# Kernel tuning notes

Hardware: AMD Instinct MI355X
Metric: run time of the kernel (lower is better)

## Reference

```python
import jax, jax.numpy as jnp
import numpy as np

N = 100000
E = 1600000
IN_FEATS = 128
N_HIDDEN = 128
N_CLASSES = 40
EPS = 1e-5


def _gconv(x, W, b, src, dst, n):
    # DGL GraphConv with norm='both': D_out^{-1/2} A D_in^{-1/2} X W (+ b), degrees clamped to >=1
    ones = jnp.ones(src.shape[0], x.dtype)
    out_deg = jnp.clip(jax.ops.segment_sum(ones, src, num_segments=n), 1.0)
    in_deg = jnp.clip(jax.ops.segment_sum(ones, dst, num_segments=n), 1.0)
    h = x * (out_deg ** -0.5)[:, None]
    agg = jax.ops.segment_sum(h[src], dst, num_segments=n)  # SpMM
    agg = agg * (in_deg ** -0.5)[:, None]
    out = agg @ W
    return out + b if b is not None else out


def setup_inputs() -> dict:
    key = jax.random.key(0)
    ks = jax.random.split(key, 16)
    s = lambda fan: 1.0 / np.sqrt(fan)
    feat = jax.random.normal(ks[0], (N, IN_FEATS), dtype=jnp.float32)
    src = jax.random.randint(ks[1], (E,), 0, N, dtype=jnp.int32)
    dst = jax.random.randint(ks[2], (E,), 0, N, dtype=jnp.int32)
    # backward convs: in_feats -> in_hidden (128->128 all layers); bias only at last layer
    Wb = jax.random.uniform(ks[3], (3, IN_FEATS, N_HIDDEN), jnp.float32, -s(IN_FEATS), s(IN_FEATS))
    bb2 = jax.random.uniform(ks[4], (N_HIDDEN,), jnp.float32, -s(IN_FEATS), s(IN_FEATS))
    # forward convs: layers 0,1 are 128->128, layer 2 is 128->40 with bias
    Wh01 = jax.random.uniform(ks[5], (2, N_HIDDEN, N_HIDDEN), jnp.float32, -s(N_HIDDEN), s(N_HIDDEN))
    W2 = jax.random.uniform(ks[6], (N_HIDDEN, N_CLASSES), jnp.float32, -s(N_HIDDEN), s(N_HIDDEN))
    b2 = jax.random.uniform(ks[7], (N_CLASSES,), jnp.float32, -s(N_HIDDEN), s(N_HIDDEN))
    # linear branch (use_linear=True), no bias
    Wl01 = jax.random.uniform(ks[8], (2, N_HIDDEN, N_HIDDEN), jnp.float32, -s(N_HIDDEN), s(N_HIDDEN))
    Wl2 = jax.random.uniform(ks[9], (N_HIDDEN, N_CLASSES), jnp.float32, -s(N_HIDDEN), s(N_HIDDEN))
    gamma = jnp.ones((2, N_HIDDEN), jnp.float32)
    beta = jnp.zeros((2, N_HIDDEN), jnp.float32)
    return {"feat": feat, "Wb": Wb, "bb2": bb2, "Wh01": Wh01, "W2": W2, "b2": b2,
            "Wl01": Wl01, "Wl2": Wl2, "gamma": gamma, "beta": beta, "src": src, "dst": dst}


def reference(feat, Wb, bb2, Wh01, W2, b2, Wl01, Wl2, gamma, beta, src, dst):
    n = feat.shape[0]
    h = feat  # dropout is identity in eval
    for i in range(3):
        last = i == 2
        # backward GraphConv on reversed graph, always applied to raw input features
        hb = _gconv(feat, Wb[i], bb2 if last else None, dst, src, n)
        h = jnp.maximum(h, hb)
        W = W2 if last else Wh01[i]
        Wl = Wl2 if last else Wl01[i]
        h = _gconv(h, W, b2 if last else None, src, dst, n) + h @ Wl
        if not last:
            mu = jnp.mean(h, axis=0)
            var = jnp.var(h, axis=0)
            h = (h - mu) * jax.lax.rsqrt(var + EPS) * gamma[i] + beta[i]
            h = jax.nn.relu(h)
    return h
```

## Files before the change

### kernel.cpp

```cpp
#include <hip/hip_runtime.h>

#define NN 100000
#define NE 1600000
#define KF 128
#define NCLS 40
#define EPSV 1e-5f
#define NBUK 391
#define TBUK 782
#define EPB 4096
#define P1B ((NE + EPB - 1) / EPB)
#define CAP 6144

typedef short bf16x8 __attribute__((ext_vector_type(8)));
typedef float f32x4 __attribute__((ext_vector_type(4)));
typedef unsigned short ushort;
typedef unsigned int uint;
typedef ushort ush8 __attribute__((ext_vector_type(8)));

static __device__ __forceinline__ int imax1(int x) { return x > 0 ? x : 1; }

static __device__ __forceinline__ ushort f2b(float f) {
  uint u = __builtin_bit_cast(uint, f);
  u += 0x7fffu + ((u >> 16) & 1u);
  return (ushort)(u >> 16);
}
static __device__ __forceinline__ float b2f(uint bits16) {
  return __builtin_bit_cast(float, bits16 << 16);
}


__global__ __launch_bounds__(256) void kb_hist(const int* __restrict__ src, const int* __restrict__ dst,
                                               int* __restrict__ gcount) {
  __shared__ int hist[TBUK];
  for (int t = threadIdx.x; t < TBUK; t += 256) hist[t] = 0;
  __syncthreads();
  int base = blockIdx.x * EPB + threadIdx.x;
#pragma unroll
  for (int i = 0; i < 16; ++i) {
    int e = base + i * 256;
    if (e < NE) {
      atomicAdd(&hist[dst[e] >> 8], 1);
      atomicAdd(&hist[NBUK + (src[e] >> 8)], 1);
    }
  }
  __syncthreads();
  for (int t = threadIdx.x; t < TBUK; t += 256)
    if (hist[t]) atomicAdd(&gcount[t], hist[t]);
}

__global__ __launch_bounds__(1024) void kb_scan(const int* __restrict__ gcount,
                                                int* __restrict__ gbase, int* __restrict__ gcur) {
  __shared__ int sm[1024];
  int t = threadIdx.x;
  int v = (t < TBUK) ? gcount[t] : 0;
  sm[t] = v;
  __syncthreads();
  for (int d = 1; d < 1024; d <<= 1) {
    int x = (t >= d) ? sm[t - d] : 0;
    __syncthreads();
    sm[t] += x;
    __syncthreads();
  }
  int excl = sm[t] - v;
  if (t <= TBUK) gbase[t] = excl;
  if (t < TBUK) gcur[t] = excl;
}

__global__ __launch_bounds__(256) void kb_place(const int* __restrict__ src, const int* __restrict__ dst,
                                                int* __restrict__ gcur,
                                                uint2* __restrict__ pairs_f, uint2* __restrict__ pairs_r) {
  __shared__ uint2 stage[EPB];
  __shared__ int hist[TBUK];
  __shared__ int sbase[TBUK];
  for (int t = threadIdx.x; t < TBUK; t += 256) hist[t] = 0;
  __syncthreads();
  int base = blockIdx.x * EPB;
  int nloc = min(EPB, NE - base);
  for (int i = threadIdx.x; i < nloc; i += 256) {
    int e = base + i;
    uint2 p;
    p.x = (uint)src[e];
    p.y = (uint)dst[e];
    stage[i] = p;
    atomicAdd(&hist[p.y >> 8], 1);
    atomicAdd(&hist[NBUK + (p.x >> 8)], 1);
  }
  __syncthreads();
  for (int t = threadIdx.x; t < TBUK; t += 256)
    sbase[t] = hist[t] ? atomicAdd(&gcur[t], hist[t]) : 0;
  __syncthreads();
  for (int i = threadIdx.x; i < nloc; i += 256) {
    uint2 p = stage[i];
    int pf = atomicAdd(&sbase[p.y >> 8], 1);
    int pr = atomicAdd(&sbase[NBUK + (p.x >> 8)], 1);
    pairs_f[pf] = make_uint2(p.y, p.x);
    pairs_r[pr - NE] = make_uint2(p.x, p.y);
  }
}

__global__ __launch_bounds__(256) void kb_build(const uint2* __restrict__ pairs_f,
                                                const uint2* __restrict__ pairs_r,
                                                const int* __restrict__ gbase,
                                                int* __restrict__ idx_f, int* __restrict__ idx_r,
                                                int* __restrict__ ptr_f, int* __restrict__ ptr_r,
                                                int* __restrict__ deg_in, int* __restrict__ deg_out) {
  __shared__ uint2 stage[CAP];
  __shared__ int deg[256];
  __shared__ int ss[256];
  __shared__ int cur[256];
  int b = blockIdx.x;
  int rev = (int)(b >= NBUK);
  int k = b - rev * NBUK;
  const uint2* pairs = rev ? pairs_r : pairs_f;
  int* idx = rev ? idx_r : idx_f;
  int* ptr = rev ? ptr_r : ptr_f;
  int* degA = rev ? deg_out : deg_in;
  int gb = gbase[b];
  int cnt = gbase[b + 1] - gb;
  int base = gb - rev * NE;
  int lo = k << 8;
  int t = threadIdx.x;
  deg[t] = 0;
  __syncthreads();
  for (int i = t; i < cnt; i += 256) {
    uint2 p = pairs[base + i];
    if (i < CAP) stage[i] = p;
    atomicAdd(&deg[(int)p.x - lo], 1);
  }
  __syncthreads();
  int dv = deg[t];
  if (lo + t < NN) degA[lo + t] = dv;
  ss[t] = dv;
  __syncthreads();
  for (int d = 1; d < 256; d <<= 1) {
    int x = (t >= d) ? ss[t - d] : 0;
    __syncthreads();
    ss[t] += x;
    __syncthreads();
  }
  int ex = ss[t] - dv;
  if (lo + t < NN) ptr[lo + t] = base + ex;
  cur[t] = ex;
  if (b == NBUK - 1 && t == 0) ptr_f[NN] = NE;
  if (b == TBUK - 1 && t == 0) ptr_r[NN] = NE;
  __syncthreads();
  for (int i = t; i < cnt; i += 256) {
    uint2 p = (i < CAP) ? stage[i] : pairs[base + i];
    int pos = atomicAdd(&cur[(int)p.x - lo], 1);
    idx[base + pos] = (int)p.y;
  }
}

__global__ void k_rsq(const int* __restrict__ deg_out, const int* __restrict__ deg_in,
                      float* __restrict__ ro, float* __restrict__ ri) {
  int i = blockIdx.x * blockDim.x + threadIdx.x;
  if (i < NN) {
    ro[i] = rsqrtf((float)imax1(deg_out[i]));
    ri[i] = rsqrtf((float)imax1(deg_in[i]));
  }
}

__global__ __launch_bounds__(256) void k_convF(const float* __restrict__ in, const float* __restrict__ ri,
                       ushort* __restrict__ out) {
  int t = blockIdx.x * blockDim.x + threadIdx.x;
  int i = t * 8;
  float w = ri[t >> 4];
  float4 a = *(const float4*)(in + i);
  float4 b = *(const float4*)(in + i + 4);
  ush8 o;
  o[0] = f2b(a.x * w); o[1] = f2b(a.y * w); o[2] = f2b(a.z * w); o[3] = f2b(a.w * w);
  o[4] = f2b(b.x * w); o[5] = f2b(b.y * w); o[6] = f2b(b.z * w); o[7] = f2b(b.w * w);
  *(ush8*)(out + i) = o;
}

#define WT_W2 (7 * 16384)
#define WT_L2 (WT_W2 + NCLS * KF)
__global__ __launch_bounds__(256) void k_convW(const float* __restrict__ Wb, const float* __restrict__ Wh01,
                       const float* __restrict__ Wl01, const float* __restrict__ W2,
                       const float* __restrict__ Wl2, ushort* __restrict__ wt) {
  int i = blockIdx.x * blockDim.x + threadIdx.x;
  float v;
  if (i < WT_W2) {
    int m = i >> 14, r = (i >> 7) & 127, k = i & 127;
    const float* srcm = (m < 3) ? (Wb + m * 16384)
                      : (m < 5) ? (Wh01 + (m - 3) * 16384)
                                : (Wl01 + (m - 5) * 16384);
    v = srcm[k * KF + r];
  } else {
    int j = i - WT_W2;
    int m2 = j / (NCLS * KF);
    int t = j - m2 * (NCLS * KF);
    int n = t >> 7, k = t & 127;
    v = (m2 ? Wl2 : W2)[k * NCLS + n];
  }
  wt[i] = f2b(v);
}

__global__ __launch_bounds__(256) void k_spmm_b(const ushort* __restrict__ in,
                      const int* __restrict__ ptr, const int* __restrict__ idx,
                      const float* __restrict__ wout, ushort* __restrict__ out) {
  int wid = (blockIdx.x * blockDim.x + threadIdx.x) >> 6;
  int lane = threadIdx.x & 63;
  if (wid >= NN) return;
  int beg = ptr[wid], end = ptr[wid + 1];
  int strm = lane >> 4;
  int c8 = (lane & 15) * 8;
  float s[8];
#pragma unroll
  for (int j = 0; j < 8; ++j) s[j] = 0.f;
  int p = beg + strm;
  for (; p + 4 < end; p += 8) {
    int u0 = idx[p], u1 = idx[p + 4];
    uint4 v0 = *(const uint4*)(in + (size_t)u0 * KF + c8);
    uint4 v1 = *(const uint4*)(in + (size_t)u1 * KF + c8);
    s[0] += b2f(v0.x & 0xffffu) + b2f(v1.x & 0xffffu);
    s[1] += b2f(v0.x >> 16)     + b2f(v1.x >> 16);
    s[2] += b2f(v0.y & 0xffffu) + b2f(v1.y & 0xffffu);
    s[3] += b2f(v0.y >> 16)     + b2f(v1.y >> 16);
    s[4] += b2f(v0.z & 0xffffu) + b2f(v1.z & 0xffffu);
    s[5] += b2f(v0.z >> 16)     + b2f(v1.z >> 16);
    s[6] += b2f(v0.w & 0xffffu) + b2f(v1.w & 0xffffu);
    s[7] += b2f(v0.w >> 16)     + b2f(v1.w >> 16);
  }
  if (p < end) {
    int u0 = idx[p];
    uint4 v0 = *(const uint4*)(in + (size_t)u0 * KF + c8);
    s[0] += b2f(v0.x & 0xffffu);
    s[1] += b2f(v0.x >> 16);
    s[2] += b2f(v0.y & 0xffffu);
    s[3] += b2f(v0.y >> 16);
    s[4] += b2f(v0.z & 0xffffu);
    s[5] += b2f(v0.z >> 16);
    s[6] += b2f(v0.w & 0xffffu);
    s[7] += b2f(v0.w >> 16);
  }
#pragma unroll
  for (int j = 0; j < 8; ++j) {
    s[j] += __shfl_xor(s[j], 16);
    s[j] += __shfl_xor(s[j], 32);
  }
  if (lane < 16) {
    float w = wout[wid];
    ush8 o;
#pragma unroll
    for (int j = 0; j < 8; ++j) o[j] = f2b(s[j] * w);
    *(ush8*)(out + (size_t)wid * KF + c8) = o;
  }
}

template <int NCT, bool DUAL, int EPI, bool HASB, bool NORMP>
__global__ __launch_bounds__(256) void k_gemm(
    const ushort* __restrict__ A1, const ushort* __restrict__ Wt1,
    const ushort* __restrict__ A2, const ushort* __restrict__ Wt2,
    const float* __restrict__ bias, const void* __restrict__ hprev,
    const float* __restrict__ ab, const float* __restrict__ rosc,
    float* __restrict__ outf, ushort* __restrict__ outb, ushort* __restrict__ outs,
    float* __restrict__ stat) {
  int lane = threadIdx.x & 63;
  int w = threadIdx.x >> 6;
  int r0 = blockIdx.x * 64 + w * 16;
  int arow = r0 + (lane & 15);
  if (arow > NN - 1) arow = NN - 1;
  int k0 = (lane >> 4) * 8;

  bf16x8 a1[4], a2[4];
#pragma unroll
  for (int ks = 0; ks < 4; ++ks) {
    a1[ks] = *(const bf16x8*)(A1 + (size_t)arow * KF + ks * 32 + k0);
    if (DUAL) a2[ks] = *(const bf16x8*)(A2 + (size_t)arow * KF + ks * 32 + k0);
  }
  f32x4 acc[NCT];
#pragma unroll
  for (int ct = 0; ct < NCT; ++ct) acc[ct] = (f32x4){0.f, 0.f, 0.f, 0.f};

#pragma unroll
  for (int ks = 0; ks < 4; ++ks) {
#pragma unroll
    for (int ct = 0; ct < NCT; ++ct) {
      int ncol = ct * 16 + (lane & 15);
      if (EPI == 2 && ncol > NCLS - 1) ncol = NCLS - 1;
      bf16x8 b1 = *(const bf16x8*)(Wt1 + (size_t)ncol * KF + ks * 32 + k0);
      acc[ct] = __builtin_amdgcn_mfma_f32_16x16x32_bf16(a1[ks], b1, acc[ct], 0, 0, 0);
      if (DUAL) {
        bf16x8 b2 = *(const bf16x8*)(Wt2 + (size_t)ncol * KF + ks * 32 + k0);
        acc[ct] = __builtin_amdgcn_mfma_f32_16x16x32_bf16(a2[ks], b2, acc[ct], 0, 0, 0);
      }
    }
  }

  int rbase = r0 + (lane >> 4) * 4;
  if constexpr (EPI == 0) {
    float rsc[4];
#pragma unroll
    for (int j = 0; j < 4; ++j) rsc[j] = rosc[min(rbase + j, NN - 1)];
#pragma unroll
    for (int ct = 0; ct < NCT; ++ct) {
      int col = ct * 16 + (lane & 15);
#pragma unroll
      for (int j = 0; j < 4; ++j) {
        int rr = rbase + j;
        if (rr >= NN) continue;
        float v = acc[ct][j];
        if (HASB) v += bias[col];
        float p;
        if (NORMP)
          p = fmaxf(0.f, b2f((uint)((const ushort*)hprev)[(size_t)rr * KF + col]) * ab[col] + ab[KF + col]);
        else
          p = ((const float*)hprev)[(size_t)rr * KF + col];
        float hv = fmaxf(p, v);
        outb[(size_t)rr * KF + col] = f2b(hv);
        outs[(size_t)rr * KF + col] = f2b(hv * rsc[j]);
      }
    }
  } else if constexpr (EPI == 1) {
    __shared__ float smS[4][128];
    __shared__ float smQ[4][128];
    float colS[NCT], colQ[NCT];
#pragma unroll
    for (int ct = 0; ct < NCT; ++ct) { colS[ct] = 0.f; colQ[ct] = 0.f; }
#pragma unroll
    for (int ct = 0; ct < NCT; ++ct) {
      int col = ct * 16 + (lane & 15);
#pragma unroll
      for (int j = 0; j < 4; ++j) {
        int rr = rbase + j;
        if (rr >= NN) continue;
        float v = acc[ct][j];
        outb[(size_t)rr * KF + col] = f2b(v);
        colS[ct] += v;
        colQ[ct] += v * v;
      }
    }
#pragma unroll
    for (int ct = 0; ct < NCT; ++ct) {
      colS[ct] += __shfl_xor(colS[ct], 16);
      colS[ct] += __shfl_xor(colS[ct], 32);
      colQ[ct] += __shfl_xor(colQ[ct], 16);
      colQ[ct] += __shfl_xor(colQ[ct], 32);
    }
    if (lane < 16) {
#pragma unroll
      for (int ct = 0; ct < NCT; ++ct) {
        smS[w][ct * 16 + lane] = colS[ct];
        smQ[w][ct * 16 + lane] = colQ[ct];
      }
    }
    __syncthreads();
    int tid = threadIdx.x;
    if (tid < 128)
      atomicAdd(&stat[tid], smS[0][tid] + smS[1][tid] + smS[2][tid] + smS[3][tid]);
    else
      atomicAdd(&stat[tid], smQ[0][tid - 128] + smQ[1][tid - 128] + smQ[2][tid - 128] + smQ[3][tid - 128]);
  } else {
#pragma unroll
    for (int ct = 0; ct < NCT; ++ct) {
      int col = ct * 16 + (lane & 15);
#pragma unroll
      for (int j = 0; j < 4; ++j) {
        int rr = rbase + j;
        if (rr >= NN) continue;
        if (col < NCLS) outf[(size_t)rr * NCLS + col] = acc[ct][j] + bias[col];
      }
    }
  }
}

__global__ void k_stats_fin(const float* __restrict__ stat, const float* __restrict__ gamma,
                            const float* __restrict__ beta, float* __restrict__ ab) {
  int c = threadIdx.x;
  float s = stat[c], q = stat[128 + c];
  float mu = s / (float)NN;
  float var = q / (float)NN - mu * mu;
  float rs = rsqrtf(var + EPSV);
  float a = gamma[c] * rs;
  ab[c] = a;
  ab[KF + c] = beta[c] - mu * a;
}

extern "C" void kernel_launch(void* const* d_in, const int* in_sizes, int n_in,
                              void* d_out, int out_size, void* d_ws, size_t ws_size,
                              hipStream_t stream) {
  const float* feat  = (const float*)d_in[0];
  const float* Wb    = (const float*)d_in[1];
  const float* bb2   = (const float*)d_in[2];
  const float* Wh01  = (const float*)d_in[3];
  const float* W2    = (const float*)d_in[4];
  const float* b2    = (const float*)d_in[5];
  const float* Wl01  = (const float*)d_in[6];
  const float* Wl2   = (const float*)d_in[7];
  const float* gamma = (const float*)d_in[8];
  const float* beta  = (const float*)d_in[9];
  const int* src = (const int*)d_in[10];
  const int* dst = (const int*)d_in[11];
  float* out = (float*)d_out;

  char* ws = (char*)d_ws;
  size_t off = 0;
  auto alloc = [&](size_t b) { size_t o = off; off += (b + 255) & ~(size_t)255; return o; };
  size_t z0 = alloc((size_t)(TBUK + 512) * 4);
  int* gcount = (int*)(ws + z0);
  float* stat = (float*)(gcount + TBUK);
  int* gbase = (int*)(ws + alloc((size_t)(TBUK + 1) * 4));
  int* gcur  = (int*)(ws + alloc((size_t)TBUK * 4));
  int* deg_out = (int*)(ws + alloc((size_t)NN * 4));
  int* deg_in  = (int*)(ws + alloc((size_t)NN * 4));
  int* ptr_f = (int*)(ws + alloc((size_t)(NN + 1) * 4));
  int* ptr_r = (int*)(ws + alloc((size_t)(NN + 1) * 4));
  int* idx_f = (int*)(ws + alloc((size_t)NE * 4));
  int* idx_r = (int*)(ws + alloc((size_t)NE * 4));
  uint2* pairs_f = (uint2*)(ws + alloc((size_t)NE * 8));
  uint2* pairs_r = (uint2*)(ws + alloc((size_t)NE * 8));
  float* ro = (float*)(ws + alloc((size_t)NN * 4));
  float* ri = (float*)(ws + alloc((size_t)NN * 4));
  ushort* featb = (ushort*)(ws + alloc((size_t)NN * KF * 2));
  ushort* aggb  = (ushort*)(ws + alloc((size_t)NN * KF * 2));
  ushort* hmaxb = (ushort*)(ws + alloc((size_t)NN * KF * 2));
  ushort* hmaxs = (ushort*)(ws + alloc((size_t)NN * KF * 2));
  float* ab = (float*)(ws + alloc((size_t)256 * 4));
  ushort* wt = (ushort*)(ws + alloc((size_t)(WT_L2 + NCLS * KF) * 2));
  ushort* t1b = featb;
  (void)ws_size;

  hipMemsetAsync(ws + z0, 0, (size_t)(TBUK + 512) * 4, stream);
  kb_hist<<<P1B, 256, 0, stream>>>(src, dst, gcount);
  kb_scan<<<1, 1024, 0, stream>>>(gcount, gbase, gcur);
  kb_place<<<P1B, 256, 0, stream>>>(src, dst, gcur, pairs_f, pairs_r);
  kb_build<<<TBUK, 256, 0, stream>>>(pairs_f, pairs_r, gbase, idx_f, idx_r,
                                     ptr_f, ptr_r, deg_in, deg_out);
  k_rsq<<<(NN + 255) / 256, 256, 0, stream>>>(deg_out, deg_in, ro, ri);
  k_convW<<<(WT_L2 + NCLS * KF + 255) / 256, 256, 0, stream>>>(Wb, Wh01, Wl01, W2, Wl2, wt);
  k_convF<<<NN * KF / 8 / 256, 256, 0, stream>>>(feat, ri, featb);

  const ushort* wtB[3] = {wt, wt + 16384, wt + 2 * 16384};
  const ushort* wtH[2] = {wt + 3 * 16384, wt + 4 * 16384};
  const ushort* wtL[2] = {wt + 5 * 16384, wt + 6 * 16384};
  const ushort* wtW2 = wt + WT_W2;
  const ushort* wtL2 = wt + WT_L2;

  int sb = (NN * 64 + 255) / 256;
  k_spmm_b<<<sb, 256, 0, stream>>>(featb, ptr_r, idx_r, ro, aggb);

  int mb = (NN + 63) / 64;
  k_gemm<8, false, 0, false, false><<<mb, 256, 0, stream>>>(
      aggb, wtB[0], nullptr, nullptr, nullptr, feat, nullptr, ro, nullptr, hmaxb, hmaxs, nullptr);
  k_spmm_b<<<sb, 256, 0, stream>>>(hmaxs, ptr_f, idx_f, ri, t1b);
  k_gemm<8, true, 1, false, false><<<mb, 256, 0, stream>>>(
      t1b, wtH[0], hmaxb, wtL[0], nullptr, nullptr, nullptr, nullptr, nullptr, hmaxb, nullptr, stat);
  k_stats_fin<<<1, 128, 0, stream>>>(stat, gamma, beta, ab);
  k_gemm<8, false, 0, false, true><<<mb, 256, 0, stream>>>(
      aggb, wtB[1], nullptr, nullptr, nullptr, hmaxb, ab, ro, nullptr, hmaxb, hmaxs, nullptr);
  k_spmm_b<<<sb, 256, 0, stream>>>(hmaxs, ptr_f, idx_f, ri, t1b);
  k_gemm<8, true, 1, false, false><<<mb, 256, 0, stream>>>(
      t1b, wtH[1], hmaxb, wtL[1], nullptr, nullptr, nullptr, nullptr, nullptr, hmaxb, nullptr, stat + 256);
  k_stats_fin<<<1, 128, 0, stream>>>(stat + 256, gamma + KF, beta + KF, ab);
  k_gemm<8, false, 0, true, true><<<mb, 256, 0, stream>>>(
      aggb, wtB[2], nullptr, nullptr, bb2, hmaxb, ab, ro, nullptr, hmaxb, hmaxs, nullptr);
  k_spmm_b<<<sb, 256, 0, stream>>>(hmaxs, ptr_f, idx_f, ri, t1b);
  k_gemm<3, true, 2, false, false><<<mb, 256, 0, stream>>>(
      t1b, wtW2, hmaxb, wtL2, b2, nullptr, nullptr, nullptr, out, nullptr, nullptr, nullptr);
}
```

Before: 821.7 us.

## Split GEMM waves across output columns and keep weight fragments in registers

The dense GEMM kernel is restructured so each of the four waves in a block covers all 64 rows but only a 32-column slice, rather than 16 rows across every column. Each wave loads its weight fragments once into registers and reuses them for four row tiles, cutting repeated weight loads. The A tiles are now read by all four waves. Because waves in a block now write rows that other waves still read as their second input, a separate hpreb buffer holds the pre-norm activations to avoid that race. For the 40-class output, half the waves do clamped work whose results are thrown away.

```diff
diff --git a/kernel.cpp b/kernel.cpp
--- a/kernel.cpp
+++ b/kernel.cpp
@@ -248,7 +248,7 @@
   }
 }
 
-template <int NCT, bool DUAL, int EPI, bool HASB, bool NORMP>
+template <int WCT, bool DUAL, int EPI, bool HASB, bool NORMP>
 __global__ __launch_bounds__(256) void k_gemm(
     const ushort* __restrict__ A1, const ushort* __restrict__ Wt1,
     const ushort* __restrict__ A2, const ushort* __restrict__ Wt2,
@@ -258,81 +258,100 @@
     float* __restrict__ stat) {
   int lane = threadIdx.x & 63;
   int w = threadIdx.x >> 6;
-  int r0 = blockIdx.x * 64 + w * 16;
-  int arow = r0 + (lane & 15);
-  if (arow > NN - 1) arow = NN - 1;
+  int r0 = blockIdx.x * 64;
+  int wcol = w * (WCT * 16);
   int k0 = (lane >> 4) * 8;
-
-  bf16x8 a1[4], a2[4];
-#pragma unroll
-  for (int ks = 0; ks < 4; ++ks) {
-    a1[ks] = *(const bf16x8*)(A1 + (size_t)arow * KF + ks * 32 + k0);
-    if (DUAL) a2[ks] = *(const bf16x8*)(A2 + (size_t)arow * KF + ks * 32 + k0);
-  }
-  f32x4 acc[NCT];
-#pragma unroll
-  for (int ct = 0; ct < NCT; ++ct) acc[ct] = (f32x4){0.f, 0.f, 0.f, 0.f};
-
-#pragma unroll
-  for (int ks = 0; ks < 4; ++ks) {
-#pragma unroll
-    for (int ct = 0; ct < NCT; ++ct) {
-      int ncol = ct * 16 + (lane & 15);
-      if (EPI == 2 && ncol > NCLS - 1) ncol = NCLS - 1;
-      bf16x8 b1 = *(const bf16x8*)(Wt1 + (size_t)ncol * KF + ks * 32 + k0);
-      acc[ct] = __builtin_amdgcn_mfma_f32_16x16x32_bf16(a1[ks], b1, acc[ct], 0, 0, 0);
-      if (DUAL) {
-        bf16x8 b2 = *(const bf16x8*)(Wt2 + (size_t)ncol * KF + ks * 32 + k0);
-        acc[ct] = __builtin_amdgcn_mfma_f32_16x16x32_bf16(a2[ks], b2, acc[ct], 0, 0, 0);
+  int l15 = lane & 15;
+  int g = lane >> 4;
+
+  bf16x8 b1[WCT][4];
+  bf16x8 b2[DUAL ? WCT : 1][DUAL ? 4 : 1];
+#pragma unroll
+  for (int ct = 0; ct < WCT; ++ct) {
+    int ncol = wcol + ct * 16 + l15;
+    if (EPI == 2) ncol = min(ncol, NCLS - 1);
+#pragma unroll
+    for (int ks = 0; ks < 4; ++ks) {
+      b1[ct][ks] = *(const bf16x8*)(Wt1 + (size_t)ncol * KF + ks * 32 + k0);
+      if (DUAL) b2[ct][ks] = *(const bf16x8*)(Wt2 + (size_t)ncol * KF + ks * 32 + k0);
+    }
+  }
+
+  f32x4 acc[4][WCT];
+#pragma unroll
+  for (int rt = 0; rt < 4; ++rt)
+#pragma unroll
+    for (int ct = 0; ct < WCT; ++ct) acc[rt][ct] = (f32x4){0.f, 0.f, 0.f, 0.f};
+
+#pragma unroll
+  for (int rt = 0; rt < 4; ++rt) {
+    int arow = min(r0 + rt * 16 + l15, NN - 1);
+    bf16x8 a1[4], a2[DUAL ? 4 : 1];
+#pragma unroll
+    for (int ks = 0; ks < 4; ++ks) {
+      a1[ks] = *(const bf16x8*)(A1 + (size_t)arow * KF + ks * 32 + k0);
+      if (DUAL) a2[ks] = *(const bf16x8*)(A2 + (size_t)arow * KF + ks * 32 + k0);
+    }
+#pragma unroll
+    for (int ks = 0; ks < 4; ++ks)
+#pragma unroll
+      for (int ct = 0; ct < WCT; ++ct) {
+        acc[rt][ct] = __builtin_amdgcn_mfma_f32_16x16x32_bf16(a1[ks], b1[ct][ks], acc[rt][ct], 0, 0, 0);
+        if (DUAL)
+          acc[rt][ct] = __builtin_amdgcn_mfma_f32_16x16x32_bf16(a2[ks], b2[ct][ks], acc[rt][ct], 0, 0, 0);
       }
-    }
-  }
-
-  int rbase = r0 + (lane >> 4) * 4;
+  }
+
   if constexpr (EPI == 0) {
-    float rsc[4];
-#pragma unroll
-    for (int j = 0; j < 4; ++j) rsc[j] = rosc[min(rbase + j, NN - 1)];
-#pragma unroll
-    for (int ct = 0; ct < NCT; ++ct) {
-      int col = ct * 16 + (lane & 15);
+#pragma unroll
+    for (int rt = 0; rt < 4; ++rt) {
+      int rbase = r0 + rt * 16 + g * 4;
 #pragma unroll
       for (int j = 0; j < 4; ++j) {
         int rr = rbase + j;
         if (rr >= NN) continue;
-        float v = acc[ct][j];
-        if (HASB) v += bias[col];
-        float p;
-        if (NORMP)
-          p = fmaxf(0.f, b2f((uint)((const ushort*)hprev)[(size_t)rr * KF + col]) * ab[col] + ab[KF + col]);
-        else
-          p = ((const float*)hprev)[(size_t)rr * KF + col];
-        float hv = fmaxf(p, v);
-        outb[(size_t)rr * KF + col] = f2b(hv);
-        outs[(size_t)rr * KF + col] = f2b(hv * rsc[j]);
+        float rs = rosc[rr];
+#pragma unroll
+        for (int ct = 0; ct < WCT; ++ct) {
+          int col = wcol + ct * 16 + l15;
+          float v = acc[rt][ct][j];
+          if (HASB) v += bias[col];
+          float p;
+          if (NORMP)
+            p = fmaxf(0.f, b2f((uint)((const ushort*)hprev)[(size_t)rr * KF + col]) * ab[col] + ab[KF + col]);
+          else
+            p = ((const float*)hprev)[(size_t)rr * KF + col];
+          float hv = fmaxf(p, v);
+          outb[(size_t)rr * KF + col] = f2b(hv);
+          outs[(size_t)rr * KF + col] = f2b(hv * rs);
+        }
       }
     }
   } else if constexpr (EPI == 1) {
-    __shared__ float smS[4][128];
-    __shared__ float smQ[4][128];
-    float colS[NCT], colQ[NCT];
-#pragma unroll
-    for (int ct = 0; ct < NCT; ++ct) { colS[ct] = 0.f; colQ[ct] = 0.f; }
-#pragma unroll
-    for (int ct = 0; ct < NCT; ++ct) {
-      int col = ct * 16 + (lane & 15);
-#pragma unroll
-      for (int j = 0; j < 4; ++j) {
-        int rr = rbase + j;
-        if (rr >= NN) continue;
-        float v = acc[ct][j];
-        outb[(size_t)rr * KF + col] = f2b(v);
-        colS[ct] += v;
-        colQ[ct] += v * v;
+    __shared__ float smS[128];
+    __shared__ float smQ[128];
+    float colS[WCT], colQ[WCT];
+#pragma unroll
+    for (int ct = 0; ct < WCT; ++ct) { colS[ct] = 0.f; colQ[ct] = 0.f; }
+#pragma unroll
+    for (int rt = 0; rt < 4; ++rt) {
+      int rbase = r0 + rt * 16 + g * 4;
+#pragma unroll
+      for (int ct = 0; ct < WCT; ++ct) {
+        int col = wcol + ct * 16 + l15;
+#pragma unroll
+        for (int j = 0; j < 4; ++j) {
+          int rr = rbase + j;
+          if (rr >= NN) continue;
+          float v = acc[rt][ct][j];
+          outb[(size_t)rr * KF + col] = f2b(v);
+          colS[ct] += v;
+          colQ[ct] += v * v;
+        }
       }
     }
 #pragma unroll
-    for (int ct = 0; ct < NCT; ++ct) {
+    for (int ct = 0; ct < WCT; ++ct) {
       colS[ct] += __shfl_xor(colS[ct], 16);
       colS[ct] += __shfl_xor(colS[ct], 32);
       colQ[ct] += __shfl_xor(colQ[ct], 16);
@@ -340,26 +359,31 @@
     }
     if (lane < 16) {
 #pragma unroll
-      for (int ct = 0; ct < NCT; ++ct) {
-        smS[w][ct * 16 + lane] = colS[ct];
-        smQ[w][ct * 16 + lane] = colQ[ct];
+      for (int ct = 0; ct < WCT; ++ct) {
+        smS[wcol + ct * 16 + lane] = colS[ct];
+        smQ[wcol + ct * 16 + lane] = colQ[ct];
       }
     }
     __syncthreads();
     int tid = threadIdx.x;
     if (tid < 128)
-      atomicAdd(&stat[tid], smS[0][tid] + smS[1][tid] + smS[2][tid] + smS[3][tid]);
+      atomicAdd(&stat[tid], smS[tid]);
     else
-      atomicAdd(&stat[tid], smQ[0][tid - 128] + smQ[1][tid - 128] + smQ[2][tid - 128] + smQ[3][tid - 128]);
+      atomicAdd(&stat[tid], smQ[tid - 128]);
   } else {
 #pragma unroll
-    for (int ct = 0; ct < NCT; ++ct) {
-      int col = ct * 16 + (lane & 15);
-#pragma unroll
-      for (int j = 0; j < 4; ++j) {
-        int rr = rbase + j;
-        if (rr >= NN) continue;
-        if (col < NCLS) outf[(size_t)rr * NCLS + col] = acc[ct][j] + bias[col];
+    for (int rt = 0; rt < 4; ++rt) {
+      int rbase = r0 + rt * 16 + g * 4;
+#pragma unroll
+      for (int ct = 0; ct < WCT; ++ct) {
+        int col = wcol + ct * 16 + l15;
+        if (col >= NCLS) continue;
+#pragma unroll
+        for (int j = 0; j < 4; ++j) {
+          int rr = rbase + j;
+          if (rr >= NN) continue;
+          outf[(size_t)rr * NCLS + col] = acc[rt][ct][j] + bias[col];
+        }
       }
     }
   }
@@ -416,6 +440,7 @@
   ushort* aggb  = (ushort*)(ws + alloc((size_t)NN * KF * 2));
   ushort* hmaxb = (ushort*)(ws + alloc((size_t)NN * KF * 2));
   ushort* hmaxs = (ushort*)(ws + alloc((size_t)NN * KF * 2));
+  ushort* hpreb = (ushort*)(ws + alloc((size_t)NN * KF * 2));
   float* ab = (float*)(ws + alloc((size_t)256 * 4));
   ushort* wt = (ushort*)(ws + alloc((size_t)(WT_L2 + NCLS * KF) * 2));
   ushort* t1b = featb;
@@ -441,21 +466,21 @@
   k_spmm_b<<<sb, 256, 0, stream>>>(featb, ptr_r, idx_r, ro, aggb);
 
   int mb = (NN + 63) / 64;
-  k_gemm<8, false, 0, false, false><<<mb, 256, 0, stream>>>(
+  k_gemm<2, false, 0, false, false><<<mb, 256, 0, stream>>>(
       aggb, wtB[0], nullptr, nullptr, nullptr, feat, nullptr, ro, nullptr, hmaxb, hmaxs, nullptr);
   k_spmm_b<<<sb, 256, 0, stream>>>(hmaxs, ptr_f, idx_f, ri, t1b);
-  k_gemm<8, true, 1, false, false><<<mb, 256, 0, stream>>>(
-      t1b, wtH[0], hmaxb, wtL[0], nullptr, nullptr, nullptr, nullptr, nullptr, hmaxb, nullptr, stat);
+  k_gemm<2, true, 1, false, false><<<mb, 256, 0, stream>>>(
+      t1b, wtH[0], hmaxb, wtL[0], nullptr, nullptr, nullptr, nullptr, nullptr, hpreb, nullptr, stat);
   k_stats_fin<<<1, 128, 0, stream>>>(stat, gamma, beta, ab);
-  k_gemm<8, false, 0, false, true><<<mb, 256, 0, stream>>>(
-      aggb, wtB[1], nullptr, nullptr, nullptr, hmaxb, ab, ro, nullptr, hmaxb, hmaxs, nullptr);
+  k_gemm<2, false, 0, false, true><<<mb, 256, 0, stream>>>(
+      aggb, wtB[1], nullptr, nullptr, nullptr, hpreb, ab, ro, nullptr, hmaxb, hmaxs, nullptr);
   k_spmm_b<<<sb, 256, 0, stream>>>(hmaxs, ptr_f, idx_f, ri, t1b);
-  k_gemm<8, true, 1, false, false><<<mb, 256, 0, stream>>>(
-      t1b, wtH[1], hmaxb, wtL[1], nullptr, nullptr, nullptr, nullptr, nullptr, hmaxb, nullptr, stat + 256);
+  k_gemm<2, true, 1, false, false><<<mb, 256, 0, stream>>>(
+      t1b, wtH[1], hmaxb, wtL[1], nullptr, nullptr, nullptr, nullptr, nullptr, hpreb, nullptr, stat + 256);
   k_stats_fin<<<1, 128, 0, stream>>>(stat + 256, gamma + KF, beta + KF, ab);
-  k_gemm<8, false, 0, true, true><<<mb, 256, 0, stream>>>(
-      aggb, wtB[2], nullptr, nullptr, bb2, hmaxb, ab, ro, nullptr, hmaxb, hmaxs, nullptr);
+  k_gemm<2, false, 0, true, true><<<mb, 256, 0, stream>>>(
+      aggb, wtB[2], nullptr, nullptr, bb2, hpreb, ab, ro, nullptr, hmaxb, hmaxs, nullptr);
   k_spmm_b<<<sb, 256, 0, stream>>>(hmaxs, ptr_f, idx_f, ri, t1b);
-  k_gemm<3, true, 2, false, false><<<mb, 256, 0, stream>>>(
+  k_gemm<2, true, 2, false, false><<<mb, 256, 0, stream>>>(
       t1b, wtW2, hmaxb, wtL2, b2, nullptr, nullptr, nullptr, out, nullptr, nullptr, nullptr);
 }
```

Result: faster. 755.0 us (-8.1%).
